# Optimization experiments

Hardware: AMD Instinct MI355X
Metric: run time of the kernel (lower is better)

The kernel has to match this reference:

```python
import jax, jax.numpy as jnp
import numpy as np
from jax import lax

V, E, H, B, S, L, T = 30000, 300, 256, 32, 256, 4, 9
H2 = 2 * H            # bidirectional encoder output / decoder hidden
DIN = 2 * H2 + L      # decoder LSTM input size


def setup_inputs() -> dict:
    key = jax.random.key(0)
    ks = jax.random.split(key, 14)
    rn = lambda k, shp, s=0.05: (jax.random.normal(k, shp, dtype=jnp.float32) * s)
    return {
        "seqs": jax.random.randint(ks[0], (B, S), 0, V, dtype=jnp.int32),
        "emb": rn(ks[1], (V, E)),
        "enc_Wih_f": rn(ks[2], (4 * H, E)),
        "enc_Whh_f": rn(ks[3], (4 * H, H)),
        "enc_b_f": rn(ks[4], (4 * H,)),
        "enc_Wih_b": rn(ks[5], (4 * H, E)),
        "enc_Whh_b": rn(ks[6], (4 * H, H)),
        "enc_b_b": rn(ks[7], (4 * H,)),
        "W_att": rn(ks[8], (H2, H2)),
        "dec_Wih": rn(ks[9], (4 * H2, DIN)),
        "dec_Whh": rn(ks[10], (4 * H2, H2)),
        "dec_b": rn(ks[11], (4 * H2,)),
        "W_tag": rn(ks[12], (T, H2)),
        "b_tag": rn(ks[13], (T,)),
    }


def _lstm_scan(x_seq, Wih, Whh, b, hidden):
    """x_seq: [S,B,Din] -> outputs [S,B,hidden]. PyTorch gate order i,f,g,o."""
    nb = x_seq.shape[1]
    h0 = jnp.zeros((nb, hidden), x_seq.dtype)
    c0 = jnp.zeros((nb, hidden), x_seq.dtype)

    def step(carry, x):
        h, c = carry
        g = x @ Wih.T + h @ Whh.T + b
        i, f, gg, o = jnp.split(g, 4, axis=-1)
        c = jax.nn.sigmoid(f) * c + jax.nn.sigmoid(i) * jnp.tanh(gg)
        h = jax.nn.sigmoid(o) * jnp.tanh(c)
        return (h, c), h

    _, hs = lax.scan(step, (h0, c0), x_seq)
    return hs


def reference(seqs, emb, enc_Wih_f, enc_Whh_f, enc_b_f, enc_Wih_b, enc_Whh_b,
              enc_b_b, W_att, dec_Wih, dec_Whh, dec_b, W_tag, b_tag):
    # embed and transpose to [S, B, E]
    x = jnp.transpose(emb[seqs], (1, 0, 2))
    # bidirectional encoder LSTM -> h: [S, B, 2H]
    h_f = _lstm_scan(x, enc_Wih_f, enc_Whh_f, enc_b_f, H)
    h_b = jnp.flip(_lstm_scan(jnp.flip(x, 0), enc_Wih_b, enc_Whh_b, enc_b_b, H), 0)
    h = jnp.concatenate([h_f, h_b], axis=-1)

    # precompute W_att @ h (same math as per-step linear in original)
    Wh = jnp.einsum('sbh,oh->sbo', h, W_att)   # [S,B,H2]

    s0 = jnp.zeros((B, H2), x.dtype)
    c0 = jnp.zeros((B, H2), x.dtype)

    def decode_level(carry, onehot):           # onehot: [L]
        def step(carry2, h_t):                 # h_t: [B,H2]
            s, c = carry2
            score = jnp.einsum('sbo,bo->bs', Wh, s)       # [B,S]
            att = jax.nn.softmax(score, axis=1)
            ctx = jnp.einsum('sbh,bs->bh', h, att)        # [B,H2]
            xin = jnp.concatenate(
                [ctx, h_t, jnp.broadcast_to(onehot, (B, L))], axis=-1)
            g = xin @ dec_Wih.T + s @ dec_Whh.T + dec_b
            i, f, gg, o = jnp.split(g, 4, axis=-1)
            c = jax.nn.sigmoid(f) * c + jax.nn.sigmoid(i) * jnp.tanh(gg)
            s = jax.nn.sigmoid(o) * jnp.tanh(c)
            return (s, c), s

        carry, outs = lax.scan(step, carry, h)  # outs: [S,B,H2]
        return carry, outs

    # state (s,c) persists across nested levels, matching the original loop
    _, all_outs = lax.scan(decode_level, (s0, c0), jnp.eye(L, dtype=x.dtype))
    # [L,S,B,H2] -> tag scores [L,S,B,T]
    return jnp.einsum('lsbh,th->lsbt', all_outs, W_tag) + b_tag
```

## Files before the change

kernel.cpp:

```cpp
#include <hip/hip_runtime.h>
#include <cstdint>
#include <cstddef>

using u16 = unsigned short;
using u32 = unsigned int;

typedef __attribute__((ext_vector_type(8))) __bf16 bf16x8;
typedef __attribute__((ext_vector_type(4))) float f32x4;
typedef __attribute__((ext_vector_type(4))) u32 u32x4;

__device__ __forceinline__ float bf2f(u16 u){
  union { u32 i; float f; } v; v.i = ((u32)u) << 16; return v.f;
}
__device__ __forceinline__ u16 f2bf(float f){
  union { float f; u32 i; } v; v.f = f;
  return (u16)((v.i + 0x7FFFu + ((v.i >> 16) & 1u)) >> 16);
}
__device__ __forceinline__ float sigm(float x){ return 1.0f / (1.0f + __expf(-x)); }
__device__ __forceinline__ f32x4 mfma16(bf16x8 a, bf16x8 b, f32x4 c){
  return __builtin_amdgcn_mfma_f32_16x16x32_bf16(a, b, c, 0, 0, 0);
}
__device__ __forceinline__ float ldin(const void* p, size_t i, bool f){
  return f ? ((const float*)p)[i] : bf2f(((const u16*)p)[i]);
}

__device__ __forceinline__ u32x4 ldx4_cg(const u16* p){
  u32x4 r;
  asm volatile("global_load_dwordx4 %0, %1, off sc0 sc1" : "=v"(r) : "v"(p) : "memory");
  return r;
}
__device__ __forceinline__ void stx4_cg(u16* p, u32x4 v){
  asm volatile("global_store_dwordx4 %0, %1, off sc0 sc1" :: "v"(p), "v"(v) : "memory");
}
__device__ __forceinline__ void st16_cg(u16* p, u32 v){
  asm volatile("global_store_short %0, %1, off sc0 sc1" :: "v"(p), "v"(v) : "memory");
}
__device__ __forceinline__ void wait_vm0(){ asm volatile("s_waitcnt vmcnt(0)" ::: "memory"); }

__device__ __forceinline__ void lbar(){
  asm volatile("s_waitcnt lgkmcnt(0)" ::: "memory");
  __builtin_amdgcn_sched_barrier(0);
  __builtin_amdgcn_s_barrier();
  __builtin_amdgcn_sched_barrier(0);
}

__device__ __forceinline__ void bar_arrive(u32* bar){
  __hip_atomic_fetch_add(bar, 1u, __ATOMIC_RELAXED, __HIP_MEMORY_SCOPE_AGENT);
}
__device__ __forceinline__ void bar_spin(u32* bar, u32 tgt){
  while (__hip_atomic_load(bar, __ATOMIC_RELAXED, __HIP_MEMORY_SCOPE_AGENT) < tgt)
    __builtin_amdgcn_s_sleep(1);
}

__global__ __launch_bounds__(256) void k_detect(const u32* __restrict__ embw, u32* __restrict__ dflag){
  int tid = threadIdx.x;
  u32 cnt = 0;
  for (int t = 0; t < 32; ++t){
    u32 w = embw[t*256 + tid];
    u32 e = (w >> 7) & 0xFFu;
    cnt += (e >= 0xC0u) ? 1u : 0u;
  }
  atomicAdd(dflag, cnt);
}


__global__ __launch_bounds__(256) void k_pack(
  const void* eWihF, const void* eWihB, const void* ebF, const void* ebB,
  const void* dWih, const void* dWhh, const void* db, const void* Wtag,
  const void* eWhhF, const void* eWhhB, const void* Watt, const void* btag,
  const u32* __restrict__ dflag,
  u16* __restrict__ WihCat, float* __restrict__ bcat, u16* __restrict__ WihH,
  u16* __restrict__ Wf, float* __restrict__ lbv, u16* __restrict__ WtagP,
  u16* __restrict__ WhhFb, u16* __restrict__ WhhBb, u16* __restrict__ Wattb,
  float* __restrict__ btagf)
{
  bool isf = (*dflag > 64u);
  long i = (long)blockIdx.x * 256 + threadIdx.x;
  if (i < 655360){
    long n = i / 320, e = i - n*320;
    WihCat[i] = (e < 300)
      ? f2bf(ldin(n < 1024 ? eWihF : eWihB, (size_t)(n & 1023)*300 + e, isf)) : (u16)0;
    return;
  }
  i -= 655360;
  if (i < 2048){ bcat[i] = ldin(i < 1024 ? ebF : ebB, (size_t)(i & 1023), isf); return; }
  i -= 2048;
  if (i < 1048576){
    long n = i >> 9, k = i & 511;
    WihH[i] = f2bf(ldin(dWih, (size_t)n*1028 + 512 + k, isf));
    return;
  }
  i -= 1048576;
  if (i < 2097152){
    long e  = i & 7;
    long ln = (i >> 3) & 63;
    long kt = (i >> 9) & 31;
    long rt = (i >> 14) & 3;
    long wgi = i >> 16;
    long n = rt*512 + wgi*16 + (ln & 15);
    long k = kt*32 + (ln >> 4)*8 + e;
    Wf[i] = f2bf((k < 512) ? ldin(dWih, (size_t)n*1028 + k, isf)
                           : ldin(dWhh, (size_t)n*512 + (k - 512), isf));
    return;
  }
  i -= 2097152;
  if (i < 8192){
    long l = i >> 11, n = i & 2047;
    lbv[i] = ldin(db, n, isf) + ldin(dWih, (size_t)n*1028 + 1024 + l, isf);
    return;
  }
  i -= 8192;
  if (i < 8192){
    long n = i >> 9, k = i & 511;
    WtagP[i] = (n < 9) ? f2bf(ldin(Wtag, (size_t)n*512 + k, isf)) : (u16)0;
    return;
  }
  i -= 8192;
  if (i < 262144){ WhhFb[i] = f2bf(ldin(eWhhF, i, isf)); return; }
  i -= 262144;
  if (i < 262144){ WhhBb[i] = f2bf(ldin(eWhhB, i, isf)); return; }
  i -= 262144;
  if (i < 262144){ Wattb[i] = f2bf(ldin(Watt, i, isf)); return; }
  i -= 262144;
  if (i < 16){ btagf[i] = (i < 9) ? ldin(btag, i, isf) : 0.f; return; }
}

__global__ __launch_bounds__(256) void k_gather(
  const int* __restrict__ seqs, const void* __restrict__ emb,
  const u32* __restrict__ dflag, u16* __restrict__ X)
{
  bool isf = (*dflag > 64u);
  int idx = blockIdx.x * 256 + threadIdx.x;
  if (idx >= 8192*320) return;
  int row = idx / 320, e = idx - row*320;
  int s = row >> 5, b = row & 31;
  int tok = seqs[b*256 + s];
  X[idx] = (e < 300) ? f2bf(ldin(emb, (size_t)tok*300 + e, isf)) : (u16)0;
}


__global__ __launch_bounds__(256) void k_gemm(
  const u16* __restrict__ A, const u16* __restrict__ B, const float* __restrict__ bias,
  u16* __restrict__ C, int M, int N, int K)
{
  int mb = blockIdx.x * 32;
  int wave = threadIdx.x >> 6, lane = threadIdx.x & 63;
  int nb = blockIdx.y * 256 + wave * 64;
  int rlo = lane & 15, klane = (lane >> 4) * 8;
  f32x4 acc[2][4];
  #pragma unroll
  for (int i = 0; i < 2; ++i)
    #pragma unroll
    for (int j = 0; j < 4; ++j) acc[i][j] = (f32x4){0,0,0,0};
  for (int kk = 0; kk < K; kk += 32){
    bf16x8 a0 = *(const bf16x8*)(A + (size_t)(mb + rlo)*K + kk + klane);
    bf16x8 a1 = *(const bf16x8*)(A + (size_t)(mb + 16 + rlo)*K + kk + klane);
    #pragma unroll
    for (int nt = 0; nt < 4; ++nt){
      bf16x8 bv = *(const bf16x8*)(B + (size_t)(nb + nt*16 + rlo)*K + kk + klane);
      acc[0][nt] = mfma16(a0, bv, acc[0][nt]);
      acc[1][nt] = mfma16(a1, bv, acc[1][nt]);
    }
  }
  int rbase = (lane >> 4) * 4;
  #pragma unroll
  for (int mt = 0; mt < 2; ++mt)
    #pragma unroll
    for (int nt = 0; nt < 4; ++nt){
      int col = nb + nt*16 + rlo;
      float badd = bias ? bias[col] : 0.0f;
      #pragma unroll
      for (int r = 0; r < 4; ++r){
        int row = mb + mt*16 + rbase + r;
        C[(size_t)row*N + col] = f2bf(acc[mt][nt][r] + badd);
      }
    }
}


__global__ __launch_bounds__(256) void k_transp(const u16* __restrict__ hglob, u16* __restrict__ hT)
{
  __shared__ u16 tile_t[64][264];
  int b = blockIdx.x >> 3, d0 = (blockIdx.x & 7) * 64;
  int t = threadIdx.x;
  for (int rr = 0; rr < 16; ++rr){
    int c = rr*256 + t;
    int j = c >> 4, dq = (c & 15) * 4;
    ushort4 ld = *(const ushort4*)(hglob + ((size_t)(j*32 + b)*512 + d0 + dq));
    tile_t[dq + 0][j] = ld.x;
    tile_t[dq + 1][j] = ld.y;
    tile_t[dq + 2][j] = ld.z;
    tile_t[dq + 3][j] = ld.w;
  }
  __syncthreads();
  for (int rr = 0; rr < 8; ++rr){
    int c = rr*256 + t;
    int d = c >> 5, jq = (c & 31) * 8;
    *(uint4*)(hT + ((size_t)(b*512 + d0 + d)*256 + jq)) = *(const uint4*)&tile_t[d][jq];
  }
}


__global__ __launch_bounds__(256, 1) void k_encoder(
  const u16* __restrict__ XW, const u16* __restrict__ WhhF, const u16* __restrict__ WhhB,
  u16* __restrict__ hglob, u16* __restrict__ hstate, u32* ctrlE)
{
  int wg = blockIdx.x;
// ... 43 lines not shown
      for (int r = 0; r < 4; ++r){
        g_lds[wave][rbase + r][cc]      = acc0[r];
        g_lds[wave][16 + rbase + r][cc] = acc1[r];
      }
    }
    __syncthreads();

    for (int e = tid; e < 512; e += 256){
      int b_ = e >> 4, jc = e & 15;
      int j = w*16 + jc;
      float pre[4];
      #pragma unroll
      for (int g2 = 0; g2 < 4; ++g2)
        pre[g2] = g_lds[g2][b_][jc] + bf2f(XW[(size_t)(srow*32 + b_)*2048 + d*1024 + g2*256 + j]);
      float iv = sigm(pre[0]), fv = sigm(pre[1]);
      float gv = tanhf(pre[2]), ov = sigm(pre[3]);
      float cv = fv * c_sh[e] + iv * gv;
      c_sh[e] = cv;
      u16 hb = f2bf(ov * tanhf(cv));
      st16_cg(hw + b_*256 + j, (u32)hb);
      __builtin_nontemporal_store(hb, hglob + (size_t)(srow*32 + b_)*512 + d*256 + j);
    }
    wait_vm0();
    __syncthreads();
    if (tid == 0){
      bar_arrive(bar);
      bar_spin(bar, (u32)(t + 1) * 16u);
    }
    __syncthreads();
  }
}


__global__ __launch_bounds__(512, 1) void k_decoder(
  const u16* __restrict__ Whb, const u16* __restrict__ hT,
  const u16* __restrict__ Wf, const u16* __restrict__ Xh, const float* __restrict__ lbv,
  u16* __restrict__ Ain,
  u16* __restrict__ aouts,
  u32* bar1, u32* bar2)
{
  extern __shared__ __align__(16) u16 ablk[];
  __shared__ float score_lds[256];
  __shared__ __align__(16) u16 att_bf[256];
  __shared__ __align__(16) u16 ctx_pack[512];
  __shared__ __align__(16) u16 spack[512];
  __shared__ float gbuf[4][16][33];
  __shared__ float c_lds[512];
  const int wg = blockIdx.x, tid = threadIdx.x;
  const int wave = tid >> 6, lane = tid & 63;
  const int q = lane >> 4, cc = lane & 15;
  c_lds[tid] = 0.0f;

  bf16x8 wh[2][16];
  #pragma unroll
  for (int rt = 0; rt < 2; ++rt)
    #pragma unroll
    for (int kt = 0; kt < 16; ++kt){
      int row = wave*32 + rt*16 + cc;
      wh[rt][kt] = *(const bf16x8*)(Whb + ((size_t)(row*32 + wg))*512 + kt*32 + q*8);
    }
  const int grt = wave >> 1, gct = wave & 1;
  const int bcol = gct*16 + cc;
  const u16* WfW = Wf + (size_t)wg*65536;
  const int pb_ = tid >> 4, pdd = tid & 15;
  const int pgj = wg*16 + pdd;
  float lb[4];
  __syncthreads();

  for (int iter = 0; iter < 1024; ++iter){
    const int l = iter >> 8, t = iter & 255;
    const u32 e = (u32)(iter + 1);
    u16* AinC = Ain + (iter & 1)*32768;
    u16* AinN = Ain + ((iter & 1) ^ 1)*32768;

    {
      int c0 = tid, c1 = tid + 512, c2 = tid + 1024, c3 = tid + 1536;
      u32x4 v0 = ldx4_cg(AinC + (c0 >> 6)*1024 + 512 + (c0 & 63)*8);
      u32x4 v1 = ldx4_cg(AinC + (c1 >> 6)*1024 + 512 + (c1 & 63)*8);
      u32x4 v2 = ldx4_cg(AinC + (c2 >> 6)*1024 + 512 + (c2 & 63)*8);
      u32x4 v3 = ldx4_cg(AinC + (c3 >> 6)*1024 + 512 + (c3 & 63)*8);
      wait_vm0();
      *(u32x4*)(ablk + (c0 >> 6)*1024 + (64 + ((c0 & 63) ^ ((c0 >> 6) & 7)))*8) = v0;
      *(u32x4*)(ablk + (c1 >> 6)*1024 + (64 + ((c1 & 63) ^ ((c1 >> 6) & 7)))*8) = v1;
      *(u32x4*)(ablk + (c2 >> 6)*1024 + (64 + ((c2 & 63) ^ ((c2 >> 6) & 7)))*8) = v2;
      *(u32x4*)(ablk + (c3 >> 6)*1024 + (64 + ((c3 & 63) ^ ((c3 >> 6) & 7)))*8) = v3;
    }
    lbar();

    if ((iter & 255) == 0){
      #pragma unroll
      for (int g = 0; g < 4; ++g) lb[g] = lbv[l*2048 + g*512 + pgj];
    }
    float xh[4];
    #pragma unroll
    for (int g = 0; g < 4; ++g) xh[g] = bf2f(Xh[(size_t)(t*32 + pb_)*2048 + g*512 + pgj]);

    {
      f32x4 sa0 = {0,0,0,0}, sa1 = {0,0,0,0};
      #pragma unroll
      for (int kt = 0; kt < 16; ++kt){
        bf16x8 sv = *(const bf16x8*)(ablk + wg*1024 + ((64 + kt*4 + q) ^ (wg & 7))*8);
        sa0 = mfma16(wh[0][kt], sv, sa0);
        sa1 = mfma16(wh[1][kt], sv, sa1);
      }
      if (cc == 0){
        #pragma unroll
        for (int r = 0; r < 4; ++r){
          score_lds[wave*32      + q*4 + r] = sa0[r];
          score_lds[wave*32 + 16 + q*4 + r] = sa1[r];
        }
      }
    }
    lbar();

    if (wave == 0){
      float x0 = score_lds[lane*4+0], x1 = score_lds[lane*4+1];
      float x2 = score_lds[lane*4+2], x3 = score_lds[lane*4+3];
      float m = fmaxf(fmaxf(x0,x1), fmaxf(x2,x3));
      #pragma unroll
      for (int off = 32; off >= 1; off >>= 1) m = fmaxf(m, __shfl_xor(m, off));
      float e0 = __expf(x0-m), e1 = __expf(x1-m), e2 = __expf(x2-m), e3 = __expf(x3-m);
      float s = e0+e1+e2+e3;
      #pragma unroll
      for (int off = 32; off >= 1; off >>= 1) s += __shfl_xor(s, off);
      float inv = 1.0f / s;
      att_bf[lane*4+0] = f2bf(e0*inv);
      att_bf[lane*4+1] = f2bf(e1*inv);
      att_bf[lane*4+2] = f2bf(e2*inv);
      att_bf[lane*4+3] = f2bf(e3*inv);
    }
    lbar();

    {
      f32x4 ca0 = {0,0,0,0}, ca1 = {0,0,0,0}, ca2 = {0,0,0,0}, ca3 = {0,0,0,0};
      #pragma unroll
      for (int jt = 0; jt < 8; ++jt){
        uint4 au = {0,0,0,0};
        if (cc == 0) au = *(const uint4*)(att_bf + jt*32 + q*8);
        bf16x8 af = *(bf16x8*)&au;
        const u16* hb = hT + ((size_t)(wg*512 + wave*64 + cc))*256 + jt*32 + q*8;
        ca0 = mfma16(af, *(const bf16x8*)(hb +  0*256), ca0);
        ca1 = mfma16(af, *(const bf16x8*)(hb + 16*256), ca1);
        ca2 = mfma16(af, *(const bf16x8*)(hb + 32*256), ca2);
        ca3 = mfma16(af, *(const bf16x8*)(hb + 48*256), ca3);
      }
      if (q == 0){
        ctx_pack[wave*64 +  0 + cc] = f2bf(ca0[0]);
        ctx_pack[wave*64 + 16 + cc] = f2bf(ca1[0]);
        ctx_pack[wave*64 + 32 + cc] = f2bf(ca2[0]);
        ctx_pack[wave*64 + 48 + cc] = f2bf(ca3[0]);
      }
    }
    lbar();

    if (wave == 0){
      u32x4 v = *(const u32x4*)(ctx_pack + lane*8);
      stx4_cg(AinC + (size_t)wg*1024 + lane*8, v);
      wait_vm0();
      if (lane == 0) bar_arrive(bar2);
    }
    f32x4 ga = {0,0,0,0};
    #pragma unroll
    for (int kt = 16; kt < 32; ++kt){
      bf16x8 wa = *(const bf16x8*)(WfW + ((grt*32 + kt)*64 + lane)*8);
      bf16x8 av = *(const bf16x8*)(ablk + bcol*1024 + ((kt*4 + q) ^ (bcol & 7))*8);
      ga = mfma16(wa, av, ga);
    }
    if (tid == 0) bar_spin(bar2, 32u*e);
    lbar();

    {
      int c0 = tid, c1 = tid + 512, c2 = tid + 1024, c3 = tid + 1536;
      u32x4 v0 = ldx4_cg(AinC + (c0 >> 6)*1024 + (c0 & 63)*8);
      u32x4 v1 = ldx4_cg(AinC + (c1 >> 6)*1024 + (c1 & 63)*8);
      u32x4 v2 = ldx4_cg(AinC + (c2 >> 6)*1024 + (c2 & 63)*8);
      u32x4 v3 = ldx4_cg(AinC + (c3 >> 6)*1024 + (c3 & 63)*8);
      wait_vm0();
      *(u32x4*)(ablk + (c0 >> 6)*1024 + (((c0 & 63) ^ ((c0 >> 6) & 7)))*8) = v0;
      *(u32x4*)(ablk + (c1 >> 6)*1024 + (((c1 & 63) ^ ((c1 >> 6) & 7)))*8) = v1;
      *(u32x4*)(ablk + (c2 >> 6)*1024 + (((c2 & 63) ^ ((c2 >> 6) & 7)))*8) = v2;
      *(u32x4*)(ablk + (c3 >> 6)*1024 + (((c3 & 63) ^ ((c3 >> 6) & 7)))*8) = v3;
    }
    lbar();

    #pragma unroll
    for (int kt = 0; kt < 16; ++kt){
      bf16x8 wa = *(const bf16x8*)(WfW + ((grt*32 + kt)*64 + lane)*8);
      bf16x8 av = *(const bf16x8*)(ablk + bcol*1024 + ((kt*4 + q) ^ (bcol & 7))*8);
      ga = mfma16(wa, av, ga);
    }
    #pragma unroll
    for (int r = 0; r < 4; ++r) gbuf[grt][q*4 + r][bcol] = ga[r];
    lbar();

    {
      float pre[4];
      #pragma unroll
      for (int g = 0; g < 4; ++g)
        pre[g] = gbuf[g][pdd][pb_] + xh[g] + lb[g];
      float iv = sigm(pre[0]), fv = sigm(pre[1]);
      float gv = tanhf(pre[2]), ov = sigm(pre[3]);
      float cv = fv * c_lds[tid] + iv * gv;
      c_lds[tid] = cv;
      spack[pb_*16 + pdd] = f2bf(ov * tanhf(cv));
    }
    lbar();

    if (wave == 0){
      u32x4 v = *(const u32x4*)(spack + lane*8);
      stx4_cg(AinN + (size_t)(lane >> 1)*1024 + 512 + wg*16 + (lane & 1)*8, v);
      wait_vm0();
      if (lane == 0) bar_arrive(bar1);
    } else if (wave == 1){
      u32x4 v = *(const u32x4*)(spack + lane*8);
      stx4_cg(aouts + ((size_t)((l*256 + t)*32) + (lane >> 1))*512 + wg*16 + (lane & 1)*8, v);
    }
    if (tid == 0) bar_spin(bar1, 32u*e);
    lbar();
  }
}


__global__ __launch_bounds__(256) void k_tag(
  const u16* __restrict__ aouts, const u16* __restrict__ WtagP, const float* __restrict__ btagf,
  const u32* __restrict__ dflag, void* __restrict__ out)
{
  bool isf = (*dflag > 64u);
  int wave = threadIdx.x >> 6, lane = threadIdx.x & 63;
  int mb = (blockIdx.x * 4 + wave) * 16;
  int cc = lane & 15, klane = (lane >> 4) * 8;
  f32x4 acc = {0,0,0,0};
  const u16* Arow = aouts + (size_t)(mb + cc)*512;
  const u16* Brow = WtagP + cc*512;
  #pragma unroll
  for (int kk = 0; kk < 512; kk += 32){
    bf16x8 av = *(const bf16x8*)(Arow + kk + klane);
    bf16x8 bv = *(const bf16x8*)(Brow + kk + klane);
    acc = mfma16(av, bv, acc);
  }
  int rbase = (lane >> 4) * 4;
  if (cc < 9){
    float bt = btagf[cc];
    #pragma unroll
    for (int r = 0; r < 4; ++r){
      int row = mb + rbase + r;
      float v = acc[r] + bt;
      if (isf) ((float*)out)[(size_t)row*9 + cc] = v;
      else     ((u16*)out)[(size_t)row*9 + cc] = f2bf(v);
    }
  }
}


extern "C" void kernel_launch(void* const* d_in, const int* in_sizes, int n_in,
                              void* d_out, int out_size, void* d_ws, size_t ws_size,
                              hipStream_t stream)
{
  (void)in_sizes; (void)n_in; (void)out_size;
  if (ws_size < 98625536ull) return;

  const int* seqs = (const int*)d_in[0];

  char* ws = (char*)d_ws;
  u32*    dflag  = (u32*)(ws + 0);
  u32*    barEF  = (u32*)(ws + 1024);
  u32*    barD1  = (u32*)(ws + 3072);
  u32*    barD2  = (u32*)(ws + 4096);
  u16*    Ain    = (u16*)(ws + 8192);
  u16*    hstate = (u16*)(ws + 139264);
  u16*    WihCat = (u16*)(ws + 263168);
  float*  bcat   = (float*)(ws + 1573888);
  u16*    WihH   = (u16*)(ws + 1582080);
  u16*    Wf     = (u16*)(ws + 3679232);
  float*  lbv    = (float*)(ws + 7873536);
  u16*    WtagP  = (u16*)(ws + 7906304);
  u16*    WhhFb  = (u16*)(ws + 7922688);
  u16*    WhhBb  = (u16*)(ws + 8446976);
  u16*    Wattb  = (u16*)(ws + 8971264);
  float*  btagf  = (float*)(ws + 9495552);
  u16*    X      = (u16*)(ws + 9496576);
  u16*    XWXh   = (u16*)(ws + 14739456);
  u16*    aouts  = (u16*)(ws + 48293888);
  u16*    hglob  = (u16*)(ws + 48293888);
  u16*    hT     = (u16*)(ws + 81848320);
  u16*    Whb    = (u16*)(ws + 90236928);

  hipMemsetAsync(d_ws, 0, 204800, stream);

  k_detect<<<1, 256, 0, stream>>>((const u32*)d_in[1], dflag);
  k_pack<<<17993, 256, 0, stream>>>(
      d_in[2], d_in[5], d_in[4], d_in[7], d_in[9], d_in[10], d_in[11], d_in[12],
      d_in[3], d_in[6], d_in[8], d_in[13], dflag,
      WihCat, bcat, WihH, Wf, lbv, WtagP, WhhFb, WhhBb, Wattb, btagf);
  k_gather<<<10240, 256, 0, stream>>>(seqs, d_in[1], dflag, X);
  k_gemm<<<dim3(256, 8), 256, 0, stream>>>(X, WihCat, bcat, XWXh, 8192, 2048, 320);
  k_encoder<<<32, 256, 0, stream>>>(XWXh, WhhFb, WhhBb, hglob, hstate, barEF);
  k_gemm<<<dim3(256, 2), 256, 0, stream>>>(hglob, Wattb, nullptr, Whb, 8192, 512, 512);
  k_gemm<<<dim3(256, 8), 256, 0, stream>>>(hglob, WihH, nullptr, XWXh, 8192, 2048, 512);
  k_transp<<<256, 256, 0, stream>>>(hglob, hT);

  k_decoder<<<32, 512, 65536, stream>>>(Whb, hT, Wf, XWXh, lbv, Ain, aouts, barD1, barD2);
  k_tag<<<512, 256, 0, stream>>>(aouts, WtagP, btagf, dflag, d_out);
}
```

Before: 22.59 ms.

## Replace persistent decoder with per-step attention and gate kernel launches

Replaces the single persistent decoder kernel, which synchronized its 32 blocks through global atomic spin barriers, with two kernels launched per timestep (attention and gate), 2048 launches in total. The cell state moves to a global buffer, and the W_att·h GEMM writes a batch-major permuted layout so each attention block reads its rows contiguously. This removes the spin-barrier latency and the register-resident weights, but adds kernel launch overhead and reloads of the weights and state from memory every step.

Measured after the change: 24.00 ms. 1.06x slower.

```diff
diff --git a/kernel.cpp b/kernel.cpp
--- a/kernel.cpp
+++ b/kernel.cpp
@@ -29,20 +29,10 @@
   asm volatile("global_load_dwordx4 %0, %1, off sc0 sc1" : "=v"(r) : "v"(p) : "memory");
   return r;
 }
-__device__ __forceinline__ void stx4_cg(u16* p, u32x4 v){
-  asm volatile("global_store_dwordx4 %0, %1, off sc0 sc1" :: "v"(p), "v"(v) : "memory");
-}
 __device__ __forceinline__ void st16_cg(u16* p, u32 v){
   asm volatile("global_store_short %0, %1, off sc0 sc1" :: "v"(p), "v"(v) : "memory");
 }
 __device__ __forceinline__ void wait_vm0(){ asm volatile("s_waitcnt vmcnt(0)" ::: "memory"); }
-
-__device__ __forceinline__ void lbar(){
-  asm volatile("s_waitcnt lgkmcnt(0)" ::: "memory");
-  __builtin_amdgcn_sched_barrier(0);
-  __builtin_amdgcn_s_barrier();
-  __builtin_amdgcn_sched_barrier(0);
-}
 
 __device__ __forceinline__ void bar_arrive(u32* bar){
   __hip_atomic_fetch_add(bar, 1u, __ATOMIC_RELAXED, __HIP_MEMORY_SCOPE_AGENT);
@@ -141,7 +131,7 @@
 
 __global__ __launch_bounds__(256) void k_gemm(
   const u16* __restrict__ A, const u16* __restrict__ B, const float* __restrict__ bias,
-  u16* __restrict__ C, int M, int N, int K)
+  u16* __restrict__ C, int M, int N, int K, int perm)
 {
   int mb = blockIdx.x * 32;
   int wave = threadIdx.x >> 6, lane = threadIdx.x & 63;
@@ -172,7 +162,8 @@
       #pragma unroll
       for (int r = 0; r < 4; ++r){
         int row = mb + mt*16 + rbase + r;
-        C[(size_t)row*N + col] = f2bf(acc[mt][nt][r] + badd);
+        int crow = perm ? ((row & 31)*256 + (row >> 5)) : row;
+        C[(size_t)crow*N + col] = f2bf(acc[mt][nt][r] + badd);
       }
     }
 }
@@ -282,191 +273,158 @@
 }
 
 
-__global__ __launch_bounds__(512, 1) void k_decoder(
-  const u16* __restrict__ Whb, const u16* __restrict__ hT,
-  const u16* __restrict__ Wf, const u16* __restrict__ Xh, const float* __restrict__ lbv,
-  u16* __restrict__ Ain,
-  u16* __restrict__ aouts,
-  u32* bar1, u32* bar2)
-{
-  extern __shared__ __align__(16) u16 ablk[];
+__global__ __launch_bounds__(512) void k_dstep_attn(
+  const u16* __restrict__ Whp,
+  const u16* __restrict__ hT,
+  u16* __restrict__ Ain, int iter)
+{
+  __shared__ __align__(16) u16 s_lds[512];
   __shared__ float score_lds[256];
   __shared__ __align__(16) u16 att_bf[256];
   __shared__ __align__(16) u16 ctx_pack[512];
-  __shared__ __align__(16) u16 spack[512];
-  __shared__ float gbuf[4][16][33];
-  __shared__ float c_lds[512];
   const int wg = blockIdx.x, tid = threadIdx.x;
   const int wave = tid >> 6, lane = tid & 63;
   const int q = lane >> 4, cc = lane & 15;
-  c_lds[tid] = 0.0f;
-
-  bf16x8 wh[2][16];
-  #pragma unroll
-  for (int rt = 0; rt < 2; ++rt)
+  u16* AinC = Ain + (iter & 1)*32768;
+
+  if (tid < 64) *(u32x4*)(s_lds + tid*8) = *(const u32x4*)(AinC + wg*1024 + 512 + tid*8);
+  __syncthreads();
+
+  {
+    const u16* WhB = Whp + (size_t)wg*131072;
+    const u16* r0 = WhB + (size_t)(wave*32 + cc)*512;
+    const u16* r1 = WhB + (size_t)(wave*32 + 16 + cc)*512;
+    f32x4 sa0 = {0,0,0,0}, sa1 = {0,0,0,0};
     #pragma unroll
     for (int kt = 0; kt < 16; ++kt){
-      int row = wave*32 + rt*16 + cc;
-      wh[rt][kt] = *(const bf16x8*)(Whb + ((size_t)(row*32 + wg))*512 + kt*32 + q*8);
-    }
+      bf16x8 sv = *(const bf16x8*)(s_lds + kt*32 + q*8);
+      bf16x8 w0 = *(const bf16x8*)(r0 + kt*32 + q*8);
+      bf16x8 w1 = *(const bf16x8*)(r1 + kt*32 + q*8);
+      sa0 = mfma16(w0, sv, sa0);
+      sa1 = mfma16(w1, sv, sa1);
+    }
+    if (cc == 0){
+      #pragma unroll
+      for (int r = 0; r < 4; ++r){
+        score_lds[wave*32      + q*4 + r] = sa0[r];
+        score_lds[wave*32 + 16 + q*4 + r] = sa1[r];
+      }
+    }
+  }
+  __syncthreads();
+
+  if (wave == 0){
+    float x0 = score_lds[lane*4+0], x1 = score_lds[lane*4+1];
+    float x2 = score_lds[lane*4+2], x3 = score_lds[lane*4+3];
+    float m = fmaxf(fmaxf(x0,x1), fmaxf(x2,x3));
+    #pragma unroll
+    for (int off = 32; off >= 1; off >>= 1) m = fmaxf(m, __shfl_xor(m, off));
+    float e0 = __expf(x0-m), e1 = __expf(x1-m), e2 = __expf(x2-m), e3 = __expf(x3-m);
+    float s = e0+e1+e2+e3;
+    #pragma unroll
+    for (int off = 32; off >= 1; off >>= 1) s += __shfl_xor(s, off);
+    float inv = 1.0f / s;
+    att_bf[lane*4+0] = f2bf(e0*inv);
+    att_bf[lane*4+1] = f2bf(e1*inv);
+    att_bf[lane*4+2] = f2bf(e2*inv);
+    att_bf[lane*4+3] = f2bf(e3*inv);
+  }
+  __syncthreads();
+
+  {
+    f32x4 ca0 = {0,0,0,0}, ca1 = {0,0,0,0}, ca2 = {0,0,0,0}, ca3 = {0,0,0,0};
+    #pragma unroll
+    for (int jt = 0; jt < 8; ++jt){
+      uint4 au = {0,0,0,0};
+      if (cc == 0) au = *(const uint4*)(att_bf + jt*32 + q*8);
+      bf16x8 af = *(bf16x8*)&au;
+      const u16* hb = hT + ((size_t)(wg*512 + wave*64 + cc))*256 + jt*32 + q*8;
+      ca0 = mfma16(af, *(const bf16x8*)(hb +  0*256), ca0);
+      ca1 = mfma16(af, *(const bf16x8*)(hb + 16*256), ca1);
+      ca2 = mfma16(af, *(const bf16x8*)(hb + 32*256), ca2);
+      ca3 = mfma16(af, *(const bf16x8*)(hb + 48*256), ca3);
+    }
+    if (q == 0){
+      ctx_pack[wave*64 +  0 + cc] = f2bf(ca0[0]);
+      ctx_pack[wave*64 + 16 + cc] = f2bf(ca1[0]);
+      ctx_pack[wave*64 + 32 + cc] = f2bf(ca2[0]);
+      ctx_pack[wave*64 + 48 + cc] = f2bf(ca3[0]);
+    }
+  }
+  __syncthreads();
+
+  if (wave == 0)
+    *(u32x4*)(AinC + (size_t)wg*1024 + lane*8) = *(const u32x4*)(ctx_pack + lane*8);
+}
+
+__global__ __launch_bounds__(512) void k_dstep_gate(
+  const u16* __restrict__ Wf, const u16* __restrict__ Xh, const float* __restrict__ lbv,
+  float* __restrict__ cstate,
+  u16* __restrict__ Ain, u16* __restrict__ aouts, int iter)
+{
+  extern __shared__ __align__(16) u16 ablk[];
+  __shared__ float gbuf[4][16][33];
+  __shared__ __align__(16) u16 spack[512];
+  const int wg = blockIdx.x, tid = threadIdx.x;
+  const int wave = tid >> 6, lane = tid & 63;
+  const int q = lane >> 4, cc = lane & 15;
+  const int l = iter >> 8, t = iter & 255;
+  u16* AinC = Ain + (iter & 1)*32768;
+  u16* AinN = Ain + ((iter & 1) ^ 1)*32768;
+
+  #pragma unroll
+  for (int i = 0; i < 8; ++i){
+    int c = tid + i*512;
+    int row = c >> 7, ch = c & 127;
+    u32x4 v = *(const u32x4*)(AinC + (size_t)row*1024 + ch*8);
+    *(u32x4*)(ablk + row*1024 + ((ch ^ (row & 7)))*8) = v;
+  }
+  __syncthreads();
+
   const int grt = wave >> 1, gct = wave & 1;
   const int bcol = gct*16 + cc;
   const u16* WfW = Wf + (size_t)wg*65536;
   const int pb_ = tid >> 4, pdd = tid & 15;
   const int pgj = wg*16 + pdd;
-  float lb[4];
-  __syncthreads();
-
-  for (int iter = 0; iter < 1024; ++iter){
-    const int l = iter >> 8, t = iter & 255;
-    const u32 e = (u32)(iter + 1);
-    u16* AinC = Ain + (iter & 1)*32768;
-    u16* AinN = Ain + ((iter & 1) ^ 1)*32768;
-
-    {
-      int c0 = tid, c1 = tid + 512, c2 = tid + 1024, c3 = tid + 1536;
-      u32x4 v0 = ldx4_cg(AinC + (c0 >> 6)*1024 + 512 + (c0 & 63)*8);
-      u32x4 v1 = ldx4_cg(AinC + (c1 >> 6)*1024 + 512 + (c1 & 63)*8);
-      u32x4 v2 = ldx4_cg(AinC + (c2 >> 6)*1024 + 512 + (c2 & 63)*8);
-      u32x4 v3 = ldx4_cg(AinC + (c3 >> 6)*1024 + 512 + (c3 & 63)*8);
-      wait_vm0();
-      *(u32x4*)(ablk + (c0 >> 6)*1024 + (64 + ((c0 & 63) ^ ((c0 >> 6) & 7)))*8) = v0;
-      *(u32x4*)(ablk + (c1 >> 6)*1024 + (64 + ((c1 & 63) ^ ((c1 >> 6) & 7)))*8) = v1;
-      *(u32x4*)(ablk + (c2 >> 6)*1024 + (64 + ((c2 & 63) ^ ((c2 >> 6) & 7)))*8) = v2;
-      *(u32x4*)(ablk + (c3 >> 6)*1024 + (64 + ((c3 & 63) ^ ((c3 >> 6) & 7)))*8) = v3;
-    }
-    lbar();
-
-    if ((iter & 255) == 0){
-      #pragma unroll
-      for (int g = 0; g < 4; ++g) lb[g] = lbv[l*2048 + g*512 + pgj];
-    }
-    float xh[4];
-    #pragma unroll
-    for (int g = 0; g < 4; ++g) xh[g] = bf2f(Xh[(size_t)(t*32 + pb_)*2048 + g*512 + pgj]);
-
-    {
-      f32x4 sa0 = {0,0,0,0}, sa1 = {0,0,0,0};
-      #pragma unroll
-      for (int kt = 0; kt < 16; ++kt){
-        bf16x8 sv = *(const bf16x8*)(ablk + wg*1024 + ((64 + kt*4 + q) ^ (wg & 7))*8);
-        sa0 = mfma16(wh[0][kt], sv, sa0);
-        sa1 = mfma16(wh[1][kt], sv, sa1);
-      }
-      if (cc == 0){
-        #pragma unroll
-        for (int r = 0; r < 4; ++r){
-          score_lds[wave*32      + q*4 + r] = sa0[r];
-          score_lds[wave*32 + 16 + q*4 + r] = sa1[r];
-        }
-      }
-    }
-    lbar();
-
-    if (wave == 0){
-      float x0 = score_lds[lane*4+0], x1 = score_lds[lane*4+1];
-      float x2 = score_lds[lane*4+2], x3 = score_lds[lane*4+3];
-      float m = fmaxf(fmaxf(x0,x1), fmaxf(x2,x3));
-      #pragma unroll
-      for (int off = 32; off >= 1; off >>= 1) m = fmaxf(m, __shfl_xor(m, off));
-      float e0 = __expf(x0-m), e1 = __expf(x1-m), e2 = __expf(x2-m), e3 = __expf(x3-m);
-      float s = e0+e1+e2+e3;
-      #pragma unroll
-      for (int off = 32; off >= 1; off >>= 1) s += __shfl_xor(s, off);
-      float inv = 1.0f / s;
-      att_bf[lane*4+0] = f2bf(e0*inv);
-      att_bf[lane*4+1] = f2bf(e1*inv);
-      att_bf[lane*4+2] = f2bf(e2*inv);
-      att_bf[lane*4+3] = f2bf(e3*inv);
-    }
-    lbar();
-
-    {
-      f32x4 ca0 = {0,0,0,0}, ca1 = {0,0,0,0}, ca2 = {0,0,0,0}, ca3 = {0,0,0,0};
-      #pragma unroll
-      for (int jt = 0; jt < 8; ++jt){
-        uint4 au = {0,0,0,0};
-        if (cc == 0) au = *(const uint4*)(att_bf + jt*32 + q*8);
-        bf16x8 af = *(bf16x8*)&au;
-        const u16* hb = hT + ((size_t)(wg*512 + wave*64 + cc))*256 + jt*32 + q*8;
-        ca0 = mfma16(af, *(const bf16x8*)(hb +  0*256), ca0);
-        ca1 = mfma16(af, *(const bf16x8*)(hb + 16*256), ca1);
-        ca2 = mfma16(af, *(const bf16x8*)(hb + 32*256), ca2);
-        ca3 = mfma16(af, *(const bf16x8*)(hb + 48*256), ca3);
-      }
-      if (q == 0){
-        ctx_pack[wave*64 +  0 + cc] = f2bf(ca0[0]);
-        ctx_pack[wave*64 + 16 + cc] = f2bf(ca1[0]);
-        ctx_pack[wave*64 + 32 + cc] = f2bf(ca2[0]);
-        ctx_pack[wave*64 + 48 + cc] = f2bf(ca3[0]);
-      }
-    }
-    lbar();
-
-    if (wave == 0){
-      u32x4 v = *(const u32x4*)(ctx_pack + lane*8);
-      stx4_cg(AinC + (size_t)wg*1024 + lane*8, v);
-      wait_vm0();
-      if (lane == 0) bar_arrive(bar2);
-    }
-    f32x4 ga = {0,0,0,0};
-    #pragma unroll
-    for (int kt = 16; kt < 32; ++kt){
-      bf16x8 wa = *(const bf16x8*)(WfW + ((grt*32 + kt)*64 + lane)*8);
-      bf16x8 av = *(const bf16x8*)(ablk + bcol*1024 + ((kt*4 + q) ^ (bcol & 7))*8);
-      ga = mfma16(wa, av, ga);
-    }
-    if (tid == 0) bar_spin(bar2, 32u*e);
-    lbar();
-
-    {
-      int c0 = tid, c1 = tid + 512, c2 = tid + 1024, c3 = tid + 1536;
-      u32x4 v0 = ldx4_cg(AinC + (c0 >> 6)*1024 + (c0 & 63)*8);
-      u32x4 v1 = ldx4_cg(AinC + (c1 >> 6)*1024 + (c1 & 63)*8);
-      u32x4 v2 = ldx4_cg(AinC + (c2 >> 6)*1024 + (c2 & 63)*8);
-      u32x4 v3 = ldx4_cg(AinC + (c3 >> 6)*1024 + (c3 & 63)*8);
-      wait_vm0();
-      *(u32x4*)(ablk + (c0 >> 6)*1024 + (((c0 & 63) ^ ((c0 >> 6) & 7)))*8) = v0;
-      *(u32x4*)(ablk + (c1 >> 6)*1024 + (((c1 & 63) ^ ((c1 >> 6) & 7)))*8) = v1;
-      *(u32x4*)(ablk + (c2 >> 6)*1024 + (((c2 & 63) ^ ((c2 >> 6) & 7)))*8) = v2;
-      *(u32x4*)(ablk + (c3 >> 6)*1024 + (((c3 & 63) ^ ((c3 >> 6) & 7)))*8) = v3;
-    }
-    lbar();
-
-    #pragma unroll
-    for (int kt = 0; kt < 16; ++kt){
-      bf16x8 wa = *(const bf16x8*)(WfW + ((grt*32 + kt)*64 + lane)*8);
-      bf16x8 av = *(const bf16x8*)(ablk + bcol*1024 + ((kt*4 + q) ^ (bcol & 7))*8);
-      ga = mfma16(wa, av, ga);
-    }
-    #pragma unroll
-    for (int r = 0; r < 4; ++r) gbuf[grt][q*4 + r][bcol] = ga[r];
-    lbar();
-
-    {
-      float pre[4];
-      #pragma unroll
-      for (int g = 0; g < 4; ++g)
-        pre[g] = gbuf[g][pdd][pb_] + xh[g] + lb[g];
-      float iv = sigm(pre[0]), fv = sigm(pre[1]);
-      float gv = tanhf(pre[2]), ov = sigm(pre[3]);
-      float cv = fv * c_lds[tid] + iv * gv;
-      c_lds[tid] = cv;
-      spack[pb_*16 + pdd] = f2bf(ov * tanhf(cv));
-    }
-    lbar();
-
-    if (wave == 0){
-      u32x4 v = *(const u32x4*)(spack + lane*8);
-      stx4_cg(AinN + (size_t)(lane >> 1)*1024 + 512 + wg*16 + (lane & 1)*8, v);
-      wait_vm0();
-      if (lane == 0) bar_arrive(bar1);
-    } else if (wave == 1){
-      u32x4 v = *(const u32x4*)(spack + lane*8);
-      stx4_cg(aouts + ((size_t)((l*256 + t)*32) + (lane >> 1))*512 + wg*16 + (lane & 1)*8, v);
-    }
-    if (tid == 0) bar_spin(bar1, 32u*e);
-    lbar();
+
+  float lb[4], xh[4];
+  #pragma unroll
+  for (int g = 0; g < 4; ++g){
+    lb[g] = lbv[l*2048 + g*512 + pgj];
+    xh[g] = bf2f(Xh[(size_t)(t*32 + pb_)*2048 + g*512 + pgj]);
+  }
+  float cold = cstate[pb_*512 + pgj];
+
+  f32x4 ga = {0,0,0,0};
+  #pragma unroll
+  for (int kt = 0; kt < 32; ++kt){
+    bf16x8 wa = *(const bf16x8*)(WfW + ((grt*32 + kt)*64 + lane)*8);
+    bf16x8 av = *(const bf16x8*)(ablk + bcol*1024 + ((kt*4 + q) ^ (bcol & 7))*8);
+    ga = mfma16(wa, av, ga);
+  }
+  #pragma unroll
+  for (int r = 0; r < 4; ++r) gbuf[grt][q*4 + r][bcol] = ga[r];
+  __syncthreads();
+
+  {
+    float pre[4];
+    #pragma unroll
+    for (int g = 0; g < 4; ++g)
+      pre[g] = gbuf[g][pdd][pb_] + xh[g] + lb[g];
+    float iv = sigm(pre[0]), fv = sigm(pre[1]);
+    float gv = tanhf(pre[2]), ov = sigm(pre[3]);
+    float cv = fv * cold + iv * gv;
+    cstate[pb_*512 + pgj] = cv;
+    spack[pb_*16 + pdd] = f2bf(ov * tanhf(cv));
+  }
+  __syncthreads();
+
+  if (wave == 0){
+    u32x4 v = *(const u32x4*)(spack + lane*8);
+    *(u32x4*)(AinN + (size_t)(lane >> 1)*1024 + 512 + wg*16 + (lane & 1)*8) = v;
+  } else if (wave == 1){
+    u32x4 v = *(const u32x4*)(spack + lane*8);
+    *(u32x4*)(aouts + ((size_t)((l*256 + t)*32) + (lane >> 1))*512 + wg*16 + (lane & 1)*8) = v;
   }
 }
 
@@ -507,35 +465,34 @@
                               hipStream_t stream)
 {
   (void)in_sizes; (void)n_in; (void)out_size;
-  if (ws_size < 98625536ull) return;
+  if (ws_size < 98632704ull) return;
 
   const int* seqs = (const int*)d_in[0];
 
   char* ws = (char*)d_ws;
   u32*    dflag  = (u32*)(ws + 0);
   u32*    barEF  = (u32*)(ws + 1024);
-  u32*    barD1  = (u32*)(ws + 3072);
-  u32*    barD2  = (u32*)(ws + 4096);
   u16*    Ain    = (u16*)(ws + 8192);
-  u16*    hstate = (u16*)(ws + 139264);
-  u16*    WihCat = (u16*)(ws + 263168);
-  float*  bcat   = (float*)(ws + 1573888);
-  u16*    WihH   = (u16*)(ws + 1582080);
-  u16*    Wf     = (u16*)(ws + 3679232);
-  float*  lbv    = (float*)(ws + 7873536);
-  u16*    WtagP  = (u16*)(ws + 7906304);
-  u16*    WhhFb  = (u16*)(ws + 7922688);
-  u16*    WhhBb  = (u16*)(ws + 8446976);
-  u16*    Wattb  = (u16*)(ws + 8971264);
-  float*  btagf  = (float*)(ws + 9495552);
-  u16*    X      = (u16*)(ws + 9496576);
-  u16*    XWXh   = (u16*)(ws + 14739456);
-  u16*    aouts  = (u16*)(ws + 48293888);
-  u16*    hglob  = (u16*)(ws + 48293888);
-  u16*    hT     = (u16*)(ws + 81848320);
-  u16*    Whb    = (u16*)(ws + 90236928);
-
-  hipMemsetAsync(d_ws, 0, 204800, stream);
+  float*  cstate = (float*)(ws + 139264);
+  u16*    hstate = (u16*)(ws + 204800);
+  u16*    WihCat = (u16*)(ws + 270336);
+  float*  bcat   = (float*)(ws + 1581056);
+  u16*    WihH   = (u16*)(ws + 1589248);
+  u16*    Wf     = (u16*)(ws + 3686400);
+  float*  lbv    = (float*)(ws + 7880704);
+  u16*    WtagP  = (u16*)(ws + 7913472);
+  u16*    WhhFb  = (u16*)(ws + 7929856);
+  u16*    WhhBb  = (u16*)(ws + 8454144);
+  u16*    Wattb  = (u16*)(ws + 8978432);
+  float*  btagf  = (float*)(ws + 9502720);
+  u16*    X      = (u16*)(ws + 9503744);
+  u16*    XWXh   = (u16*)(ws + 14746624);
+  u16*    aouts  = (u16*)(ws + 48301056);
+  u16*    hglob  = (u16*)(ws + 48301056);
+  u16*    hT     = (u16*)(ws + 81855488);
+  u16*    Whp    = (u16*)(ws + 90244096);
+
+  hipMemsetAsync(d_ws, 0, 270336, stream);
 
   k_detect<<<1, 256, 0, stream>>>((const u32*)d_in[1], dflag);
   k_pack<<<17993, 256, 0, stream>>>(
@@ -543,12 +500,16 @@
       d_in[3], d_in[6], d_in[8], d_in[13], dflag,
       WihCat, bcat, WihH, Wf, lbv, WtagP, WhhFb, WhhBb, Wattb, btagf);
   k_gather<<<10240, 256, 0, stream>>>(seqs, d_in[1], dflag, X);
-  k_gemm<<<dim3(256, 8), 256, 0, stream>>>(X, WihCat, bcat, XWXh, 8192, 2048, 320);
+  k_gemm<<<dim3(256, 8), 256, 0, stream>>>(X, WihCat, bcat, XWXh, 8192, 2048, 320, 0);
   k_encoder<<<32, 256, 0, stream>>>(XWXh, WhhFb, WhhBb, hglob, hstate, barEF);
-  k_gemm<<<dim3(256, 2), 256, 0, stream>>>(hglob, Wattb, nullptr, Whb, 8192, 512, 512);
-  k_gemm<<<dim3(256, 8), 256, 0, stream>>>(hglob, WihH, nullptr, XWXh, 8192, 2048, 512);
+  k_gemm<<<dim3(256, 2), 256, 0, stream>>>(hglob, Wattb, nullptr, Whp, 8192, 512, 512, 1);
+  k_gemm<<<dim3(256, 8), 256, 0, stream>>>(hglob, WihH, nullptr, XWXh, 8192, 2048, 512, 0);
   k_transp<<<256, 256, 0, stream>>>(hglob, hT);
 
-  k_decoder<<<32, 512, 65536, stream>>>(Whb, hT, Wf, XWXh, lbv, Ain, aouts, barD1, barD2);
+  for (int it = 0; it < 1024; ++it){
+    k_dstep_attn<<<32, 512, 0, stream>>>(Whp, hT, Ain, it);
+    k_dstep_gate<<<32, 512, 65536, stream>>>(Wf, XWXh, lbv, cstate, Ain, aouts, it);
+  }
+
   k_tag<<<512, 256, 0, stream>>>(aouts, WtagP, btagf, dflag, d_out);
 }
```

## Run decoder on 16 workgroups of 1024 threads with fewer grid barrier participants

Applied to the files above, without the earlier changes.

The persistent decoder moves from 32 workgroups of 512 threads to 16 workgroups of 1024 threads. Each workgroup now handles two batch rows for attention and 32 hidden units for the gate GEMM, with the Wf packing and LDS buffers resized to match. The attention weights (W_att·h) are no longer held in registers but are read from a batch-major permuted layout written by the GEMM's new perm option. The aim is to halve the number of participants in the per-step cross-workgroup barriers, in exchange for global reloads of the attention weights every step and less total compute parallelism.

New measurement: 57.13 ms. 153% more time.

```diff
diff --git a/kernel.cpp b/kernel.cpp
--- a/kernel.cpp
+++ b/kernel.cpp
@@ -95,9 +95,11 @@
     long e  = i & 7;
     long ln = (i >> 3) & 63;
     long kt = (i >> 9) & 31;
-    long rt = (i >> 14) & 3;
-    long wgi = i >> 16;
-    long n = rt*512 + wgi*16 + (ln & 15);
+    long rt = (i >> 14) & 7;
+    long wgi = i >> 17;
+    long rl = rt*16 + (ln & 15);
+    long g2 = rl >> 5, d = rl & 31;
+    long n = g2*512 + wgi*32 + d;
     long k = kt*32 + (ln >> 4)*8 + e;
     Wf[i] = f2bf((k < 512) ? ldin(dWih, (size_t)n*1028 + k, isf)
                            : ldin(dWhh, (size_t)n*512 + (k - 512), isf));
@@ -141,7 +143,7 @@
 
 __global__ __launch_bounds__(256) void k_gemm(
   const u16* __restrict__ A, const u16* __restrict__ B, const float* __restrict__ bias,
-  u16* __restrict__ C, int M, int N, int K)
+  u16* __restrict__ C, int M, int N, int K, int perm)
 {
   int mb = blockIdx.x * 32;
   int wave = threadIdx.x >> 6, lane = threadIdx.x & 63;
@@ -172,7 +174,8 @@
       #pragma unroll
       for (int r = 0; r < 4; ++r){
         int row = mb + mt*16 + rbase + r;
-        C[(size_t)row*N + col] = f2bf(acc[mt][nt][r] + badd);
+        int crow = perm ? ((row & 31)*256 + (row >> 5)) : row;
+        C[(size_t)crow*N + col] = f2bf(acc[mt][nt][r] + badd);
       }
     }
 }
@@ -282,39 +285,32 @@
 }
 
 
-__global__ __launch_bounds__(512, 1) void k_decoder(
-  const u16* __restrict__ Whb, const u16* __restrict__ hT,
+__global__ __launch_bounds__(1024, 1) void k_decoder(
+  const u16* __restrict__ Whp, const u16* __restrict__ hT,
   const u16* __restrict__ Wf, const u16* __restrict__ Xh, const float* __restrict__ lbv,
   u16* __restrict__ Ain,
   u16* __restrict__ aouts,
   u32* bar1, u32* bar2)
 {
   extern __shared__ __align__(16) u16 ablk[];
-  __shared__ float score_lds[256];
-  __shared__ __align__(16) u16 att_bf[256];
-  __shared__ __align__(16) u16 ctx_pack[512];
-  __shared__ __align__(16) u16 spack[512];
-  __shared__ float gbuf[4][16][33];
-  __shared__ float c_lds[512];
+  __shared__ float score_lds[512];
+  __shared__ __align__(16) u16 att_bf[512];
+  __shared__ __align__(16) u16 ctx_pack[1024];
+  __shared__ __align__(16) u16 spack[1024];
+  __shared__ float gbuf[128][33];
+  __shared__ float c_lds[1024];
   const int wg = blockIdx.x, tid = threadIdx.x;
   const int wave = tid >> 6, lane = tid & 63;
   const int q = lane >> 4, cc = lane & 15;
-  c_lds[tid] = 0.0f;
-
-  bf16x8 wh[2][16];
-  #pragma unroll
-  for (int rt = 0; rt < 2; ++rt)
-    #pragma unroll
-    for (int kt = 0; kt < 16; ++kt){
-      int row = wave*32 + rt*16 + cc;
-      wh[rt][kt] = *(const bf16x8*)(Whb + ((size_t)(row*32 + wg))*512 + kt*32 + q*8);
-    }
+  const int bb = wave >> 3, aw = wave & 7;
+  const int batt = wg*2 + bb;
   const int grt = wave >> 1, gct = wave & 1;
   const int bcol = gct*16 + cc;
-  const u16* WfW = Wf + (size_t)wg*65536;
-  const int pb_ = tid >> 4, pdd = tid & 15;
-  const int pgj = wg*16 + pdd;
+  const u16* WfW = Wf + (size_t)wg*131072;
+  const int pb_ = tid >> 5, pdd = tid & 31;
+  const int pgj = wg*32 + pdd;
   float lb[4];
+  c_lds[tid] = 0.0f;
   __syncthreads();
 
   for (int iter = 0; iter < 1024; ++iter){
@@ -324,16 +320,12 @@
     u16* AinN = Ain + ((iter & 1) ^ 1)*32768;
 
     {
-      int c0 = tid, c1 = tid + 512, c2 = tid + 1024, c3 = tid + 1536;
+      int c0 = tid, c1 = tid + 1024;
       u32x4 v0 = ldx4_cg(AinC + (c0 >> 6)*1024 + 512 + (c0 & 63)*8);
       u32x4 v1 = ldx4_cg(AinC + (c1 >> 6)*1024 + 512 + (c1 & 63)*8);
-      u32x4 v2 = ldx4_cg(AinC + (c2 >> 6)*1024 + 512 + (c2 & 63)*8);
-      u32x4 v3 = ldx4_cg(AinC + (c3 >> 6)*1024 + 512 + (c3 & 63)*8);
       wait_vm0();
       *(u32x4*)(ablk + (c0 >> 6)*1024 + (64 + ((c0 & 63) ^ ((c0 >> 6) & 7)))*8) = v0;
       *(u32x4*)(ablk + (c1 >> 6)*1024 + (64 + ((c1 & 63) ^ ((c1 >> 6) & 7)))*8) = v1;
-      *(u32x4*)(ablk + (c2 >> 6)*1024 + (64 + ((c2 & 63) ^ ((c2 >> 6) & 7)))*8) = v2;
-      *(u32x4*)(ablk + (c3 >> 6)*1024 + (64 + ((c3 & 63) ^ ((c3 >> 6) & 7)))*8) = v3;
     }
     lbar();
 
@@ -346,26 +338,30 @@
     for (int g = 0; g < 4; ++g) xh[g] = bf2f(Xh[(size_t)(t*32 + pb_)*2048 + g*512 + pgj]);
 
     {
+      const u16* r0 = Whp + ((size_t)(batt*256 + aw*32 + cc))*512;
+      const u16* r1 = r0 + 16*512;
       f32x4 sa0 = {0,0,0,0}, sa1 = {0,0,0,0};
       #pragma unroll
       for (int kt = 0; kt < 16; ++kt){
-        bf16x8 sv = *(const bf16x8*)(ablk + wg*1024 + ((64 + kt*4 + q) ^ (wg & 7))*8);
-        sa0 = mfma16(wh[0][kt], sv, sa0);
-        sa1 = mfma16(wh[1][kt], sv, sa1);
+        bf16x8 sv = *(const bf16x8*)(ablk + batt*1024 + ((64 + kt*4 + q) ^ (batt & 7))*8);
+        bf16x8 w0 = *(const bf16x8*)(r0 + kt*32 + q*8);
+        bf16x8 w1 = *(const bf16x8*)(r1 + kt*32 + q*8);
+        sa0 = mfma16(w0, sv, sa0);
+        sa1 = mfma16(w1, sv, sa1);
       }
       if (cc == 0){
         #pragma unroll
         for (int r = 0; r < 4; ++r){
-          score_lds[wave*32      + q*4 + r] = sa0[r];
-          score_lds[wave*32 + 16 + q*4 + r] = sa1[r];
+          score_lds[bb*256 + aw*32      + q*4 + r] = sa0[r];
+          score_lds[bb*256 + aw*32 + 16 + q*4 + r] = sa1[r];
         }
       }
     }
     lbar();
 
-    if (wave == 0){
-      float x0 = score_lds[lane*4+0], x1 = score_lds[lane*4+1];
-      float x2 = score_lds[lane*4+2], x3 = score_lds[lane*4+3];
+    if (aw == 0){
+      float x0 = score_lds[bb*256 + lane*4+0], x1 = score_lds[bb*256 + lane*4+1];
+      float x2 = score_lds[bb*256 + lane*4+2], x3 = score_lds[bb*256 + lane*4+3];
       float m = fmaxf(fmaxf(x0,x1), fmaxf(x2,x3));
       #pragma unroll
       for (int off = 32; off >= 1; off >>= 1) m = fmaxf(m, __shfl_xor(m, off));
@@ -374,10 +370,10 @@
       #pragma unroll
       for (int off = 32; off >= 1; off >>= 1) s += __shfl_xor(s, off);
       float inv = 1.0f / s;
-      att_bf[lane*4+0] = f2bf(e0*inv);
-      att_bf[lane*4+1] = f2bf(e1*inv);
-      att_bf[lane*4+2] = f2bf(e2*inv);
-      att_bf[lane*4+3] = f2bf(e3*inv);
+      att_bf[bb*256 + lane*4+0] = f2bf(e0*inv);
+      att_bf[bb*256 + lane*4+1] = f2bf(e1*inv);
+      att_bf[bb*256 + lane*4+2] = f2bf(e2*inv);
+      att_bf[bb*256 + lane*4+3] = f2bf(e3*inv);
     }
     lbar();
 
@@ -386,29 +382,25 @@
       #pragma unroll
       for (int jt = 0; jt < 8; ++jt){
         uint4 au = {0,0,0,0};
-        if (cc == 0) au = *(const uint4*)(att_bf + jt*32 + q*8);
+        if (cc == 0) au = *(const uint4*)(att_bf + bb*256 + jt*32 + q*8);
         bf16x8 af = *(bf16x8*)&au;
-        const u16* hb = hT + ((size_t)(wg*512 + wave*64 + cc))*256 + jt*32 + q*8;
+        const u16* hb = hT + ((size_t)(batt*512 + aw*64 + cc))*256 + jt*32 + q*8;
         ca0 = mfma16(af, *(const bf16x8*)(hb +  0*256), ca0);
         ca1 = mfma16(af, *(const bf16x8*)(hb + 16*256), ca1);
         ca2 = mfma16(af, *(const bf16x8*)(hb + 32*256), ca2);
         ca3 = mfma16(af, *(const bf16x8*)(hb + 48*256), ca3);
       }
       if (q == 0){
-        ctx_pack[wave*64 +  0 + cc] = f2bf(ca0[0]);
-        ctx_pack[wave*64 + 16 + cc] = f2bf(ca1[0]);
-        ctx_pack[wave*64 + 32 + cc] = f2bf(ca2[0]);
-        ctx_pack[wave*64 + 48 + cc] = f2bf(ca3[0]);
-      }
-    }
-    lbar();
-
-    if (wave == 0){
-      u32x4 v = *(const u32x4*)(ctx_pack + lane*8);
-      stx4_cg(AinC + (size_t)wg*1024 + lane*8, v);
-      wait_vm0();
-      if (lane == 0) bar_arrive(bar2);
-    }
+        ctx_pack[bb*512 + aw*64 +  0 + cc] = f2bf(ca0[0]);
+        ctx_pack[bb*512 + aw*64 + 16 + cc] = f2bf(ca1[0]);
+        ctx_pack[bb*512 + aw*64 + 32 + cc] = f2bf(ca2[0]);
+        ctx_pack[bb*512 + aw*64 + 48 + cc] = f2bf(ca3[0]);
+      }
+    }
+    lbar();
+
+    if (aw == 0)
+      stx4_cg(AinC + (size_t)batt*1024 + lane*8, *(const u32x4*)(ctx_pack + bb*512 + lane*8));
     f32x4 ga = {0,0,0,0};
     #pragma unroll
     for (int kt = 16; kt < 32; ++kt){
@@ -416,20 +408,21 @@
       bf16x8 av = *(const bf16x8*)(ablk + bcol*1024 + ((kt*4 + q) ^ (bcol & 7))*8);
       ga = mfma16(wa, av, ga);
     }
-    if (tid == 0) bar_spin(bar2, 32u*e);
-    lbar();
-
-    {
-      int c0 = tid, c1 = tid + 512, c2 = tid + 1024, c3 = tid + 1536;
+    if (aw == 0) wait_vm0();
+    lbar();
+    if (tid == 0){
+      bar_arrive(bar2);
+      bar_spin(bar2, 16u*e);
+    }
+    lbar();
+
+    {
+      int c0 = tid, c1 = tid + 1024;
       u32x4 v0 = ldx4_cg(AinC + (c0 >> 6)*1024 + (c0 & 63)*8);
       u32x4 v1 = ldx4_cg(AinC + (c1 >> 6)*1024 + (c1 & 63)*8);
-      u32x4 v2 = ldx4_cg(AinC + (c2 >> 6)*1024 + (c2 & 63)*8);
-      u32x4 v3 = ldx4_cg(AinC + (c3 >> 6)*1024 + (c3 & 63)*8);
       wait_vm0();
       *(u32x4*)(ablk + (c0 >> 6)*1024 + (((c0 & 63) ^ ((c0 >> 6) & 7)))*8) = v0;
       *(u32x4*)(ablk + (c1 >> 6)*1024 + (((c1 & 63) ^ ((c1 >> 6) & 7)))*8) = v1;
-      *(u32x4*)(ablk + (c2 >> 6)*1024 + (((c2 & 63) ^ ((c2 >> 6) & 7)))*8) = v2;
-      *(u32x4*)(ablk + (c3 >> 6)*1024 + (((c3 & 63) ^ ((c3 >> 6) & 7)))*8) = v3;
     }
     lbar();
 
@@ -440,32 +433,37 @@
       ga = mfma16(wa, av, ga);
     }
     #pragma unroll
-    for (int r = 0; r < 4; ++r) gbuf[grt][q*4 + r][bcol] = ga[r];
+    for (int r = 0; r < 4; ++r) gbuf[grt*16 + q*4 + r][bcol] = ga[r];
     lbar();
 
     {
       float pre[4];
       #pragma unroll
       for (int g = 0; g < 4; ++g)
-        pre[g] = gbuf[g][pdd][pb_] + xh[g] + lb[g];
+        pre[g] = gbuf[g*32 + pdd][pb_] + xh[g] + lb[g];
       float iv = sigm(pre[0]), fv = sigm(pre[1]);
       float gv = tanhf(pre[2]), ov = sigm(pre[3]);
       float cv = fv * c_lds[tid] + iv * gv;
       c_lds[tid] = cv;
-      spack[pb_*16 + pdd] = f2bf(ov * tanhf(cv));
-    }
-    lbar();
-
-    if (wave == 0){
-      u32x4 v = *(const u32x4*)(spack + lane*8);
-      stx4_cg(AinN + (size_t)(lane >> 1)*1024 + 512 + wg*16 + (lane & 1)*8, v);
+      spack[tid] = f2bf(ov * tanhf(cv));
+    }
+    lbar();
+
+    if (wave < 2){
+      int c = tid;
+      stx4_cg(AinN + (size_t)(c >> 2)*1024 + 512 + wg*32 + (c & 3)*8,
+              *(const u32x4*)(spack + c*8));
       wait_vm0();
-      if (lane == 0) bar_arrive(bar1);
-    } else if (wave == 1){
-      u32x4 v = *(const u32x4*)(spack + lane*8);
-      stx4_cg(aouts + ((size_t)((l*256 + t)*32) + (lane >> 1))*512 + wg*16 + (lane & 1)*8, v);
-    }
-    if (tid == 0) bar_spin(bar1, 32u*e);
+    } else if (wave < 4){
+      int c = tid - 128;
+      stx4_cg(aouts + ((size_t)((l*256 + t)*32) + (c >> 2))*512 + wg*32 + (c & 3)*8,
+              *(const u32x4*)(spack + c*8));
+    }
+    lbar();
+    if (tid == 0){
+      bar_arrive(bar1);
+      bar_spin(bar1, 16u*e);
+    }
     lbar();
   }
 }
@@ -533,7 +531,7 @@
   u16*    aouts  = (u16*)(ws + 48293888);
   u16*    hglob  = (u16*)(ws + 48293888);
   u16*    hT     = (u16*)(ws + 81848320);
-  u16*    Whb    = (u16*)(ws + 90236928);
+  u16*    Whp    = (u16*)(ws + 90236928);
 
   hipMemsetAsync(d_ws, 0, 204800, stream);
 
@@ -543,12 +541,12 @@
       d_in[3], d_in[6], d_in[8], d_in[13], dflag,
       WihCat, bcat, WihH, Wf, lbv, WtagP, WhhFb, WhhBb, Wattb, btagf);
   k_gather<<<10240, 256, 0, stream>>>(seqs, d_in[1], dflag, X);
-  k_gemm<<<dim3(256, 8), 256, 0, stream>>>(X, WihCat, bcat, XWXh, 8192, 2048, 320);
+  k_gemm<<<dim3(256, 8), 256, 0, stream>>>(X, WihCat, bcat, XWXh, 8192, 2048, 320, 0);
   k_encoder<<<32, 256, 0, stream>>>(XWXh, WhhFb, WhhBb, hglob, hstate, barEF);
-  k_gemm<<<dim3(256, 2), 256, 0, stream>>>(hglob, Wattb, nullptr, Whb, 8192, 512, 512);
-  k_gemm<<<dim3(256, 8), 256, 0, stream>>>(hglob, WihH, nullptr, XWXh, 8192, 2048, 512);
+  k_gemm<<<dim3(256, 2), 256, 0, stream>>>(hglob, Wattb, nullptr, Whp, 8192, 512, 512, 1);
+  k_gemm<<<dim3(256, 8), 256, 0, stream>>>(hglob, WihH, nullptr, XWXh, 8192, 2048, 512, 0);
   k_transp<<<256, 256, 0, stream>>>(hglob, hT);
 
-  k_decoder<<<32, 512, 65536, stream>>>(Whb, hT, Wf, XWXh, lbv, Ain, aouts, barD1, barD2);
+  k_decoder<<<16, 1024, 65536, stream>>>(Whp, hT, Wf, XWXh, lbv, Ain, aouts, barD1, barD2);
   k_tag<<<512, 256, 0, stream>>>(aouts, WtagP, btagf, dflag, d_out);
 }
```
